# Performance work log

Hardware: AMD Instinct MI355X
Metric: run time of the kernel (lower is better)

## Reference

```python
import jax, jax.numpy as jnp
import numpy as np

T, B, H = 2048, 8, 1024


def setup_inputs() -> dict:
    key = jax.random.key(0)
    ks = jax.random.split(key, 4)
    scale = 1.0 / np.sqrt(H)
    x = jax.random.normal(ks[0], (T, B, H), dtype=jnp.float32)
    W_q = jax.random.normal(ks[1], (H, H), dtype=jnp.float32) * scale
    b_q = jnp.zeros((H,), dtype=jnp.float32)
    beta_raw = jax.random.normal(ks[2], (H,), dtype=jnp.float32)
    W_fc = jax.random.normal(ks[3], (H, H), dtype=jnp.float32) * scale
    b_fc = jnp.zeros((H,), dtype=jnp.float32)
    return {"x": x, "W_q": W_q, "b_q": b_q, "beta_raw": beta_raw,
            "W_fc": W_fc, "b_fc": b_fc}


def reference(x, W_q, b_q, beta_raw, W_fc, b_fc):
    # Per-neuron learned leak in (0,1)
    beta = jax.nn.sigmoid(beta_raw)  # (H,)
    # Input (q) projection: (T,B,H) @ (H,H)^T
    q = jnp.einsum('tbh,oh->tbo', x, W_q) + b_q  # (T,B,H)
    # Leaky integration m_t = beta * m_{t-1} + q_t as an associative scan over T
    a = jnp.broadcast_to(beta, q.shape)  # (T,B,H)

    def combine(c1, c2):
        a1, m1 = c1
        a2, m2 = c2
        return (a1 * a2, a2 * m1 + m2)

    _, m = jax.lax.associative_scan(combine, (a, q), axis=0)  # (T,B,H)
    # Linear + ReLU
    h = jnp.einsum('tbh,oh->tbo', m, W_fc) + b_fc
    return jax.nn.relu(h)
```

## Files before the change

kernel.cpp:

```cpp
#include <hip/hip_runtime.h>
#include <stdint.h>

typedef unsigned short u16;
typedef __bf16 bf16x8 __attribute__((ext_vector_type(8)));
typedef float f32x4 __attribute__((ext_vector_type(4)));

__device__ __forceinline__ u16 f2bf(float f) {
  union { float f; uint32_t u; } x; x.f = f;
  uint32_t u = x.u;
  u += 0x7fffu + ((u >> 16) & 1u);
  return (u16)(u >> 16);
}
__device__ __forceinline__ float bf2f(uint32_t lo16) {
  union { uint32_t u; float f; } x; x.u = lo16 << 16; return x.f;
}

__device__ __forceinline__ void async_load16(const u16* g, u16* l) {
  __builtin_amdgcn_global_load_lds(
      (const __attribute__((address_space(1))) void*)g,
      (__attribute__((address_space(3))) void*)l,
      16, 0, 0);
}

__global__ __launch_bounds__(256) void prep_all(const float* __restrict__ x,
                                                const float* __restrict__ Wq,
                                                const float* __restrict__ Wfc,
                                                const float* __restrict__ braw,
                                                u16* __restrict__ xb,
                                                u16* __restrict__ wqb,
                                                u16* __restrict__ wfcb,
                                                float* __restrict__ beta) {
  int gid = blockIdx.x * 256 + threadIdx.x;
  if (gid < 1024) beta[gid] = 1.0f / (1.0f + expf(-braw[gid]));
  if (gid < 131072) {
    const int HH = 1024 * 1024;
    int i = gid * 16;
    const float* src = (i < HH) ? (Wq + i) : (Wfc + (i - HH));
    u16* dst = (i < HH) ? (wqb + i) : (wfcb + (i - HH));
#pragma unroll
    for (int c = 0; c < 4; c++) {
      float4 v = *(const float4*)(src + c * 4);
      ushort4 o = {f2bf(v.x), f2bf(v.y), f2bf(v.z), f2bf(v.w)};
      *(ushort4*)(dst + c * 4) = o;
    }
  }
  {
    int i = gid * 8;
    float4 a = *(const float4*)(x + i);
    float4 b = *(const float4*)(x + i + 4);
    ushort4 o0 = {f2bf(a.x), f2bf(a.y), f2bf(a.z), f2bf(a.w)};
    ushort4 o1 = {f2bf(b.x), f2bf(b.y), f2bf(b.z), f2bf(b.w)};
    *(ushort4*)(xb + i) = o0;
    *(ushort4*)(xb + i + 4) = o1;
  }
}

template <int RELU, int OUTBF, int CARRY>
__global__ __launch_bounds__(512, 2) void gemm256(const u16* __restrict__ A,
                                                  const u16* __restrict__ B,
                                                  const float* __restrict__ bias,
                                                  void* __restrict__ Cout,
                                                  const float* __restrict__ beta_arr,
                                                  float* __restrict__ carry_out,
                                                  int M, int N, int K) {
  __shared__ u16 lds[4][2][256 * 32];

  const int tid  = threadIdx.x;
  const int lane = tid & 63;
  const int wid  = tid >> 6;
  const int wr   = (wid >> 2) * 128;
  const int wc   = (wid & 3) * 64;

  const int bid    = blockIdx.x;
  const int xcd    = bid & 7;
  const int idx    = bid >> 3;
  const int tile_m = ((xcd << 3) | (idx >> 2)) * 256;
  const int tile_n = (idx & 3) * 256;

  const int srow    = tid >> 2;
  const int schunk  = (tid & 3) ^ ((srow >> 1) & 3);
  const u16* gA = A + (size_t)(tile_m + srow) * K + schunk * 8;
  const u16* gB = B + (size_t)(tile_n + srow) * K + schunk * 8;
  const size_t half_stride = (size_t)128 * K;

#define STAGE(slot, kt)                                                   \
  do {                                                                    \
    const size_t k0 = (size_t)(kt) * 32;                                  \
    async_load16(gA + k0,               &lds[slot][0][wid * 512]);        \
    async_load16(gA + k0 + half_stride, &lds[slot][0][4096 + wid * 512]); \
    async_load16(gB + k0,               &lds[slot][1][wid * 512]);        \
    async_load16(gB + k0 + half_stride, &lds[slot][1][4096 + wid * 512]); \
  } while (0)

  f32x4 acc[8][4];
#pragma unroll
  for (int i = 0; i < 8; i++)
#pragma unroll
    for (int j = 0; j < 4; j++) acc[i][j] = (f32x4){0.f, 0.f, 0.f, 0.f};

  const int lrow = lane & 15;
  const int kq   = lane >> 4;
  const int kc   = (lrow >> 1) & 3;
  const int coff = ((kq ^ kc) << 3);

  const int NKT = K >> 5;

  STAGE(0, 0);
  if (NKT > 1) STAGE(1, 1);
  if (NKT > 2) STAGE(2, 2);
  if (NKT > 2)      asm volatile("s_waitcnt vmcnt(8)" ::: "memory");
  else if (NKT > 1) asm volatile("s_waitcnt vmcnt(4)" ::: "memory");
  else              asm volatile("s_waitcnt vmcnt(0)" ::: "memory");
  __builtin_amdgcn_s_barrier();

  for (int kt = 0; kt < NKT; ++kt) {
    const int slot = kt & 3;
    const u16* As = &lds[slot][0][0];
    const u16* Bs = &lds[slot][1][0];

    bf16x8 a[8], b[4];
#pragma unroll
    for (int i = 0; i < 8; i++)
      a[i] = *(const bf16x8*)&As[(wr + i * 16 + lrow) * 32 + coff];
#pragma unroll
    for (int j = 0; j < 4; j++)
      b[j] = *(const bf16x8*)&Bs[(wc + j * 16 + lrow) * 32 + coff];

    if (kt + 3 < NKT) STAGE((kt + 3) & 3, kt + 3);

    __builtin_amdgcn_s_setprio(1);
#pragma unroll
    for (int i = 0; i < 8; i++)
#pragma unroll
      for (int j = 0; j < 4; j++)
        acc[i][j] = __builtin_amdgcn_mfma_f32_16x16x32_bf16(a[i], b[j], acc[i][j], 0, 0, 0);
    __builtin_amdgcn_s_setprio(0);

    const int ahead = NKT - 1 - kt;
    if (ahead >= 3) {
      asm volatile("s_waitcnt vmcnt(8)" ::: "memory");
      __builtin_amdgcn_s_barrier();
    } else if (ahead == 2) {
      asm volatile("s_waitcnt vmcnt(4)" ::: "memory");
      __builtin_amdgcn_s_barrier();
    } else if (ahead == 1) {
      asm volatile("s_waitcnt vmcnt(0)" ::: "memory");
      __builtin_amdgcn_s_barrier();
    }
  }
#undef STAGE

  const int crow = (lane >> 4) << 2;
  const int ccol = lane & 15;
#pragma unroll
  for (int i = 0; i < 8; i++) {
#pragma unroll
    for (int j = 0; j < 4; j++) {
      const int gm = tile_m + wr + i * 16 + crow;
      const int gn = tile_n + wc + j * 16 + ccol;
      const float bv = bias[gn];
#pragma unroll
      for (int r = 0; r < 4; r++) {
        float v = acc[i][j][r] + bv;
        if (RELU) v = fmaxf(v, 0.f);
        if (OUTBF) ((u16*)Cout)[(size_t)(gm + r) * N + gn] = f2bf(v);
        else       ((float*)Cout)[(size_t)(gm + r) * N + gn] = v;
      }
    }
  }

  if (CARRY) {
    float* ps = (float*)&lds[0][0][0];
    const int W   = wr >> 7;
    const int kap = lane >> 5;
#pragma unroll
    for (int j = 0; j < 4; j++) {
      const int gn = tile_n + wc + j * 16 + ccol;
      const float bv = bias[gn];
      const float b1 = beta_arr[gn];
      const float b2 = b1 * b1;
      const float b4 = b2 * b2, b8 = b4 * b4, b16 = b8 * b8;
      const float scale = W ? (kap ? 1.0f : b1) : (kap ? b16 : b16 * b1);
#pragma unroll
      for (int r = 0; r < 4; r++) {
        float Hn = acc[0][j][r] + bv;
#pragma unroll
        for (int i = 1; i < 8; i++) Hn = fmaf(b2, Hn, acc[i][j][r] + bv);
        float P = scale * Hn;
        P += __shfl_xor(P, 32);
        if (lane < 32) {
          const int bb = ((lane >> 4) << 2) + r;
          ps[W * 2048 + bb * 256 + wc + j * 16 + ccol] = P;
        }
      }
    }
    __syncthreads();
    {
      const int bb = tid >> 6;
      const int h4 = (tid & 63) << 2;
      float4 lo = *(float4*)&ps[bb * 256 + h4];
      float4 hi = *(float4*)&ps[2048 + bb * 256 + h4];
      float4 s  = make_float4(lo.x + hi.x, lo.y + hi.y, lo.z + hi.z, lo.w + hi.w);
      const int seg = tile_m >> 8;
      *(float4*)&carry_out[(size_t)seg * 8192 + bb * 1024 + tile_n + h4] = s;
    }
  }
}

#define NCH 8192
#define SEG 32
#define NSEG 64

__global__ __launch_bounds__(256) void scan_fuse(const uint2* __restrict__ qb,
                                                 const float4* __restrict__ carry4,
                                                 const float* __restrict__ beta_arr,
                                                 uint2* __restrict__ mb) {
  const int tid = blockIdx.x * 256 + threadIdx.x;
  const int seg = tid >> 11;
  const int cq  = tid & 2047;
  const int h0  = (cq * 4) & 1023;
  const float b0 = beta_arr[h0], b1 = beta_arr[h0 + 1];
  const float b2 = beta_arr[h0 + 2], b3 = beta_arr[h0 + 3];
  float s0 = b0, s1 = b1, s2 = b2, s3 = b3;
#pragma unroll
  for (int i = 0; i < 5; i++) { s0 *= s0; s1 *= s1; s2 *= s2; s3 *= s3; }
  float m0 = 0.f, m1 = 0.f, m2 = 0.f, m3 = 0.f;
  const float4* cp = carry4 + cq;
  for (int s = 0; s < seg; s++) {
    float4 c = cp[(size_t)s * 2048];
    m0 = fmaf(s0, m0, c.x); m1 = fmaf(s1, m1, c.y);
    m2 = fmaf(s2, m2, c.z); m3 = fmaf(s3, m3, c.w);
  }
  const uint2* p = qb + (size_t)seg * SEG * 2048 + cq;
  uint2* o = mb + (size_t)seg * SEG * 2048 + cq;
#pragma unroll 8
  for (int t = 0; t < SEG; t++) {
    uint2 v = p[(size_t)t * 2048];
    m0 = fmaf(b0, m0, bf2f(v.x & 0xffffu));
    m1 = fmaf(b1, m1, bf2f(v.x >> 16));
    m2 = fmaf(b2, m2, bf2f(v.y & 0xffffu));
    m3 = fmaf(b3, m3, bf2f(v.y >> 16));
    uint2 w;
    w.x = (uint32_t)f2bf(m0) | ((uint32_t)f2bf(m1) << 16);
    w.y = (uint32_t)f2bf(m2) | ((uint32_t)f2bf(m3) << 16);
    o[(size_t)t * 2048] = w;
  }
}

extern "C" void kernel_launch(void* const* d_in, const int* in_sizes, int n_in,
                              void* d_out, int out_size, void* d_ws, size_t ws_size,
                              hipStream_t stream) {
  const float* x        = (const float*)d_in[0];
  const float* W_q      = (const float*)d_in[1];
  const float* b_q      = (const float*)d_in[2];
  const float* beta_raw = (const float*)d_in[3];
  const float* W_fc     = (const float*)d_in[4];
  const float* b_fc     = (const float*)d_in[5];

  const int H = 1024;
  const int M = 2048 * 8;
  const size_t MH = (size_t)M * H;

  char* ws = (char*)d_ws;
  u16* x_bf    = (u16*)ws;  ws += MH * 2;
  u16* q_bf    = (u16*)ws;  ws += MH * 2;
  u16* m_bf    = (u16*)ws;  ws += MH * 2;
  u16* wq_bf   = (u16*)ws;  ws += (size_t)H * H * 2;
  u16* wfc_bf  = (u16*)ws;  ws += (size_t)H * H * 2;
  float* beta  = (float*)ws; ws += 4096;
  float* carry = (float*)ws; ws += (size_t)NSEG * NCH * 4;

  prep_all<<<(int)(MH / 8 / 256), 256, 0, stream>>>(x, W_q, W_fc, beta_raw,
                                                    x_bf, wq_bf, wfc_bf, beta);

  gemm256<0, 1, 1><<<256, 512, 0, stream>>>(x_bf, wq_bf, b_q, q_bf,
                                            beta, carry, M, H, H);

  scan_fuse<<<NSEG * (NCH / 4) / 256, 256, 0, stream>>>((const uint2*)q_bf,
                                                        (const float4*)carry, beta,
                                                        (uint2*)m_bf);

  gemm256<1, 0, 0><<<256, 512, 0, stream>>>(m_bf, wfc_bf, b_fc, d_out,
                                            beta, nullptr, M, H, H);
}
```

Measured before the change: 234.4 us.

## Fuse local scan into first GEMM epilogue and carry fixup into second GEMM's A-load

The first GEMM now computes the within-tile leaky scan in its epilogue, using shuffles and LDS to combine the two wave-row halves, and writes segment-local m values and per-segment carries. A tiny ffold kernel turns the carries into segment prefix states. The second GEMM loads A through registers and applies the carry correction (beta^t * F) before writing to LDS. This removes the separate full-tensor scan pass over q, at the cost of a register-staged A path, extra bpow/Fbuf loads inside the GEMM main loop, and a serial 64-step fold run by only 8 blocks.

```diff
diff --git a/kernel.cpp b/kernel.cpp
--- a/kernel.cpp
+++ b/kernel.cpp
@@ -13,6 +13,15 @@
 }
 __device__ __forceinline__ float bf2f(uint32_t lo16) {
   union { uint32_t u; float f; } x; x.u = lo16 << 16; return x.f;
+}
+__device__ __forceinline__ float bfhi(uint32_t u) {
+  union { uint32_t u; float f; } x; x.u = u & 0xffff0000u; return x.f;
+}
+__device__ __forceinline__ uint32_t fixpair(uint32_t m, float p0, float p1,
+                                            float F0, float F1) {
+  float e0 = fmaf(p0, F0, bf2f(m & 0xffffu));
+  float e1 = fmaf(p1, F1, bfhi(m));
+  return (uint32_t)f2bf(e0) | ((uint32_t)f2bf(e1) << 16);
 }
 
 __device__ __forceinline__ void async_load16(const u16* g, u16* l) {
@@ -29,9 +38,16 @@
                                                 u16* __restrict__ xb,
                                                 u16* __restrict__ wqb,
                                                 u16* __restrict__ wfcb,
-                                                float* __restrict__ beta) {
+                                                float* __restrict__ beta,
+                                                float* __restrict__ bpow) {
   int gid = blockIdx.x * 256 + threadIdx.x;
-  if (gid < 1024) beta[gid] = 1.0f / (1.0f + expf(-braw[gid]));
+  if (gid < 1024) {
+    float b = 1.0f / (1.0f + expf(-braw[gid]));
+    beta[gid] = b;
+    float w = b;
+#pragma unroll 1
+    for (int p = 1; p <= 32; p++) { bpow[p * 1024 + gid] = w; w *= b; }
+  }
   if (gid < 131072) {
     const int HH = 1024 * 1024;
     int i = gid * 16;
@@ -55,14 +71,13 @@
   }
 }
 
-template <int RELU, int OUTBF, int CARRY>
-__global__ __launch_bounds__(512, 2) void gemm256(const u16* __restrict__ A,
-                                                  const u16* __restrict__ B,
-                                                  const float* __restrict__ bias,
-                                                  void* __restrict__ Cout,
-                                                  const float* __restrict__ beta_arr,
-                                                  float* __restrict__ carry_out,
-                                                  int M, int N, int K) {
+__global__ __launch_bounds__(512, 2) void gemm_scan(const u16* __restrict__ A,
+                                                    const u16* __restrict__ B,
+                                                    const float* __restrict__ bias,
+                                                    u16* __restrict__ Cout,
+                                                    const float* __restrict__ beta_arr,
+                                                    float* __restrict__ carry_out,
+                                                    int M, int N, int K) {
   __shared__ u16 lds[4][2][256 * 32];
 
   const int tid  = threadIdx.x;
@@ -152,6 +167,242 @@
 
   const int crow = (lane >> 4) << 2;
   const int ccol = lane & 15;
+  const int c4   = lane >> 4;
+  const int kap  = c4 >> 1;
+  const int Wh   = wr >> 7;
+  float* sm15 = (float*)&lds[0][0][0];
+
+#pragma unroll
+  for (int j = 0; j < 4; j++) {
+    const int gn = tile_n + wc + j * 16 + ccol;
+    const float bv = bias[gn];
+    const float be = beta_arr[gn];
+    const float be2 = be * be;
+#pragma unroll
+    for (int r = 0; r < 4; r++) {
+      float S[8], R[8];
+      S[0] = acc[0][j][r] + bv;
+#pragma unroll
+      for (int i = 1; i < 8; i++) S[i] = fmaf(be2, S[i - 1], acc[i][j][r] + bv);
+#pragma unroll
+      for (int i = 0; i < 8; i++) R[i] = __shfl_xor(S[i], 32);
+      acc[0][j][r] = kap ? fmaf(be, R[0], S[0]) : S[0];
+#pragma unroll
+      for (int i = 1; i < 8; i++)
+        acc[i][j][r] = fmaf(be, kap ? R[i] : R[i - 1], S[i]);
+    }
+  }
+  if (Wh == 0 && kap == 1) {
+#pragma unroll
+    for (int j = 0; j < 4; j++)
+#pragma unroll
+      for (int r = 0; r < 4; r++) {
+        const int bb = ((c4 << 2) + r) & 7;
+        sm15[bb * 256 + wc + j * 16 + ccol] = acc[7][j][r];
+      }
+  }
+  __syncthreads();
+  if (Wh == 1) {
+#pragma unroll
+    for (int j = 0; j < 4; j++) {
+      const int hl = wc + j * 16 + ccol;
+      const float be = beta_arr[tile_n + hl];
+      const float be2 = be * be;
+#pragma unroll
+      for (int r = 0; r < 4; r++) {
+        const int bb = ((c4 << 2) + r) & 7;
+        const float v = sm15[bb * 256 + hl];
+        float f = kap ? be2 : be;
+#pragma unroll
+        for (int i = 0; i < 8; i++) {
+          acc[i][j][r] = fmaf(f, v, acc[i][j][r]);
+          f *= be2;
+        }
+      }
+    }
+  }
+#pragma unroll
+  for (int i = 0; i < 8; i++) {
+#pragma unroll
+    for (int j = 0; j < 4; j++) {
+      const int gm = tile_m + wr + i * 16 + crow;
+      const int gn = tile_n + wc + j * 16 + ccol;
+#pragma unroll
+      for (int r = 0; r < 4; r++)
+        Cout[(size_t)(gm + r) * N + gn] = f2bf(acc[i][j][r]);
+    }
+  }
+  if (Wh == 1 && kap == 1) {
+    const int seg = tile_m >> 8;
+#pragma unroll
+    for (int j = 0; j < 4; j++) {
+      const int hl = wc + j * 16 + ccol;
+#pragma unroll
+      for (int r = 0; r < 4; r++) {
+        const int bb = ((c4 << 2) + r) & 7;
+        carry_out[(size_t)seg * 8192 + bb * 1024 + tile_n + hl] = acc[7][j][r];
+      }
+    }
+  }
+}
+
+__global__ __launch_bounds__(256) void ffold(const float4* __restrict__ carry4,
+                                             const float* __restrict__ bpow,
+                                             float4* __restrict__ Fbuf) {
+  const int cq = blockIdx.x * 256 + threadIdx.x;
+  const int hq = cq & 255;
+  const float4 b32 = *(const float4*)&bpow[32 * 1024 + hq * 4];
+  float4 F = make_float4(0.f, 0.f, 0.f, 0.f);
+  for (int s = 0; s < 64; s++) {
+    Fbuf[(size_t)s * 2048 + cq] = F;
+    float4 c = carry4[(size_t)s * 2048 + cq];
+    F.x = fmaf(b32.x, F.x, c.x);
+    F.y = fmaf(b32.y, F.y, c.y);
+    F.z = fmaf(b32.z, F.z, c.z);
+    F.w = fmaf(b32.w, F.w, c.w);
+  }
+}
+
+__global__ __launch_bounds__(512, 2) void gemm_fix(const u16* __restrict__ A,
+                                                   const u16* __restrict__ B,
+                                                   const float* __restrict__ bias,
+                                                   float* __restrict__ Cout,
+                                                   const float* __restrict__ bpow,
+                                                   const float* __restrict__ Fbuf,
+                                                   int M, int N, int K) {
+  __shared__ u16 lds[4][2][256 * 32];
+
+  const int tid  = threadIdx.x;
+  const int lane = tid & 63;
+  const int wid  = tid >> 6;
+  const int wr   = (wid >> 2) * 128;
+  const int wc   = (wid & 3) * 64;
+
+  const int bid    = blockIdx.x;
+  const int xcd    = bid & 7;
+  const int idx    = bid >> 3;
+  const int tile_m = ((xcd << 3) | (idx >> 2)) * 256;
+  const int tile_n = (idx & 3) * 256;
+
+  const int srow    = tid >> 2;
+  const int schunk  = (tid & 3) ^ ((srow >> 1) & 3);
+  const int t0      = srow >> 3;
+  const int bb      = srow & 7;
+  const int seg     = tile_m >> 8;
+
+  const u16*   gA2 = A + (size_t)(tile_m + srow) * K + schunk * 8;
+  const u16*   gB  = B + (size_t)(tile_n + srow) * K + schunk * 8;
+  const float* pb0 = bpow + (size_t)(t0 + 1) * 1024 + schunk * 8;
+  const float* fb0 = Fbuf + (size_t)seg * 8192 + bb * 1024 + schunk * 8;
+  const size_t half_stride = (size_t)128 * K;
+
+  struct ARegs { uint4 m0, m1; float4 p0l, p0h, p1l, p1h, fl, fh; };
+  ARegs rA, rB;
+
+#define STAGE_B2(slot, kt)                                                \
+  do {                                                                    \
+    const size_t k0 = (size_t)(kt) * 32;                                  \
+    async_load16(gB + k0,               &lds[slot][1][wid * 512]);        \
+    async_load16(gB + k0 + half_stride, &lds[slot][1][4096 + wid * 512]); \
+  } while (0)
+
+#define LOADA(R, kt)                                                      \
+  do {                                                                    \
+    const size_t o = (size_t)(kt) * 32;                                   \
+    (R).m0  = *(const uint4*)(gA2 + o);                                   \
+    (R).m1  = *(const uint4*)(gA2 + o + half_stride);                     \
+    (R).p0l = *(const float4*)(pb0 + o);                                  \
+    (R).p0h = *(const float4*)(pb0 + o + 4);                              \
+    (R).p1l = *(const float4*)(pb0 + o + 16384);                          \
+    (R).p1h = *(const float4*)(pb0 + o + 16388);                          \
+    (R).fl  = *(const float4*)(fb0 + o);                                  \
+    (R).fh  = *(const float4*)(fb0 + o + 4);                              \
+  } while (0)
+
+#define FIXWRITE(slot, R)                                                 \
+  do {                                                                    \
+    uint4 w0, w1;                                                         \
+    w0.x = fixpair((R).m0.x, (R).p0l.x, (R).p0l.y, (R).fl.x, (R).fl.y);   \
+    w0.y = fixpair((R).m0.y, (R).p0l.z, (R).p0l.w, (R).fl.z, (R).fl.w);   \
+    w0.z = fixpair((R).m0.z, (R).p0h.x, (R).p0h.y, (R).fh.x, (R).fh.y);   \
+    w0.w = fixpair((R).m0.w, (R).p0h.z, (R).p0h.w, (R).fh.z, (R).fh.w);   \
+    w1.x = fixpair((R).m1.x, (R).p1l.x, (R).p1l.y, (R).fl.x, (R).fl.y);   \
+    w1.y = fixpair((R).m1.y, (R).p1l.z, (R).p1l.w, (R).fl.z, (R).fl.w);   \
+    w1.z = fixpair((R).m1.z, (R).p1h.x, (R).p1h.y, (R).fh.x, (R).fh.y);   \
+    w1.w = fixpair((R).m1.w, (R).p1h.z, (R).p1h.w, (R).fh.z, (R).fh.w);   \
+    *(uint4*)&lds[slot][0][tid * 8]        = w0;                          \
+    *(uint4*)&lds[slot][0][4096 + tid * 8] = w1;                          \
+  } while (0)
+
+  f32x4 acc[8][4];
+#pragma unroll
+  for (int i = 0; i < 8; i++)
+#pragma unroll
+    for (int j = 0; j < 4; j++) acc[i][j] = (f32x4){0.f, 0.f, 0.f, 0.f};
+
+  const int lrow = lane & 15;
+  const int kq   = lane >> 4;
+  const int kc   = (lrow >> 1) & 3;
+  const int coff = ((kq ^ kc) << 3);
+
+  const int NKT = K >> 5;
+
+  LOADA(rA, 0);
+  LOADA(rB, 1);
+  STAGE_B2(0, 0);
+  STAGE_B2(1, 1);
+  STAGE_B2(2, 2);
+  asm volatile("s_waitcnt vmcnt(0)" ::: "memory");
+  FIXWRITE(0, rA);
+  FIXWRITE(1, rB);
+  LOADA(rA, 2);
+  asm volatile("s_waitcnt lgkmcnt(0)" ::: "memory");
+  __builtin_amdgcn_sched_barrier(0);
+  __builtin_amdgcn_s_barrier();
+
+#define ITER(kt, RW, RL)                                                      \
+  do {                                                                       \
+    const int slot = (kt) & 3;                                               \
+    bf16x8 a[8], b[4];                                                       \
+    _Pragma("unroll")                                                        \
+    for (int i = 0; i < 8; i++)                                              \
+      a[i] = *(const bf16x8*)&lds[slot][0][(wr + i * 16 + lrow) * 32 + coff];\
+    _Pragma("unroll")                                                        \
+    for (int j = 0; j < 4; j++)                                              \
+      b[j] = *(const bf16x8*)&lds[slot][1][(wc + j * 16 + lrow) * 32 + coff];\
+    if ((kt) + 3 < NKT) STAGE_B2(((kt) + 3) & 3, (kt) + 3);                  \
+    if ((kt) + 2 < NKT) {                                                    \
+      if ((kt) + 3 < NKT) asm volatile("s_waitcnt vmcnt(2)" ::: "memory");   \
+      else                asm volatile("s_waitcnt vmcnt(0)" ::: "memory");   \
+      FIXWRITE(((kt) + 2) & 3, RW);                                          \
+    }                                                                        \
+    if ((kt) + 3 < NKT) LOADA(RL, (kt) + 3);                                 \
+    __builtin_amdgcn_s_setprio(1);                                           \
+    _Pragma("unroll")                                                        \
+    for (int i = 0; i < 8; i++)                                              \
+      _Pragma("unroll")                                                      \
+      for (int j = 0; j < 4; j++)                                            \
+        acc[i][j] = __builtin_amdgcn_mfma_f32_16x16x32_bf16(a[i], b[j],      \
+                                                            acc[i][j], 0, 0, 0); \
+    __builtin_amdgcn_s_setprio(0);                                           \
+    if ((kt) < NKT - 1) {                                                    \
+      asm volatile("s_waitcnt lgkmcnt(0)" ::: "memory");                     \
+      __builtin_amdgcn_sched_barrier(0);                                     \
+      __builtin_amdgcn_s_barrier();                                          \
+    }                                                                        \
+  } while (0)
+
+  for (int kt = 0; kt < NKT; kt += 2) {
+    ITER(kt, rA, rB);
+    ITER(kt + 1, rB, rA);
+  }
+#undef ITER
+#undef FIXWRITE
+#undef LOADA
+#undef STAGE_B2
+
+  const int crow = (lane >> 4) << 2;
+  const int ccol = lane & 15;
 #pragma unroll
   for (int i = 0; i < 8; i++) {
 #pragma unroll
@@ -162,88 +413,10 @@
 #pragma unroll
       for (int r = 0; r < 4; r++) {
         float v = acc[i][j][r] + bv;
-        if (RELU) v = fmaxf(v, 0.f);
-        if (OUTBF) ((u16*)Cout)[(size_t)(gm + r) * N + gn] = f2bf(v);
-        else       ((float*)Cout)[(size_t)(gm + r) * N + gn] = v;
+        v = fmaxf(v, 0.f);
+        Cout[(size_t)(gm + r) * N + gn] = v;
       }
     }
-  }
-
-  if (CARRY) {
-    float* ps = (float*)&lds[0][0][0];
-    const int W   = wr >> 7;
-    const int kap = lane >> 5;
-#pragma unroll
-    for (int j = 0; j < 4; j++) {
-      const int gn = tile_n + wc + j * 16 + ccol;
-      const float bv = bias[gn];
-      const float b1 = beta_arr[gn];
-      const float b2 = b1 * b1;
-      const float b4 = b2 * b2, b8 = b4 * b4, b16 = b8 * b8;
-      const float scale = W ? (kap ? 1.0f : b1) : (kap ? b16 : b16 * b1);
-#pragma unroll
-      for (int r = 0; r < 4; r++) {
-        float Hn = acc[0][j][r] + bv;
-#pragma unroll
-        for (int i = 1; i < 8; i++) Hn = fmaf(b2, Hn, acc[i][j][r] + bv);
-        float P = scale * Hn;
-        P += __shfl_xor(P, 32);
-        if (lane < 32) {
-          const int bb = ((lane >> 4) << 2) + r;
-          ps[W * 2048 + bb * 256 + wc + j * 16 + ccol] = P;
-        }
-      }
-    }
-    __syncthreads();
-    {
-      const int bb = tid >> 6;
-      const int h4 = (tid & 63) << 2;
-      float4 lo = *(float4*)&ps[bb * 256 + h4];
-      float4 hi = *(float4*)&ps[2048 + bb * 256 + h4];
-      float4 s  = make_float4(lo.x + hi.x, lo.y + hi.y, lo.z + hi.z, lo.w + hi.w);
-      const int seg = tile_m >> 8;
-      *(float4*)&carry_out[(size_t)seg * 8192 + bb * 1024 + tile_n + h4] = s;
-    }
-  }
-}
-
-#define NCH 8192
-#define SEG 32
-#define NSEG 64
-
-__global__ __launch_bounds__(256) void scan_fuse(const uint2* __restrict__ qb,
-                                                 const float4* __restrict__ carry4,
-                                                 const float* __restrict__ beta_arr,
-                                                 uint2* __restrict__ mb) {
-  const int tid = blockIdx.x * 256 + threadIdx.x;
-  const int seg = tid >> 11;
-  const int cq  = tid & 2047;
-  const int h0  = (cq * 4) & 1023;
-  const float b0 = beta_arr[h0], b1 = beta_arr[h0 + 1];
-  const float b2 = beta_arr[h0 + 2], b3 = beta_arr[h0 + 3];
-  float s0 = b0, s1 = b1, s2 = b2, s3 = b3;
-#pragma unroll
-  for (int i = 0; i < 5; i++) { s0 *= s0; s1 *= s1; s2 *= s2; s3 *= s3; }
-  float m0 = 0.f, m1 = 0.f, m2 = 0.f, m3 = 0.f;
-  const float4* cp = carry4 + cq;
-  for (int s = 0; s < seg; s++) {
-    float4 c = cp[(size_t)s * 2048];
-    m0 = fmaf(s0, m0, c.x); m1 = fmaf(s1, m1, c.y);
-    m2 = fmaf(s2, m2, c.z); m3 = fmaf(s3, m3, c.w);
-  }
-  const uint2* p = qb + (size_t)seg * SEG * 2048 + cq;
-  uint2* o = mb + (size_t)seg * SEG * 2048 + cq;
-#pragma unroll 8
-  for (int t = 0; t < SEG; t++) {
-    uint2 v = p[(size_t)t * 2048];
-    m0 = fmaf(b0, m0, bf2f(v.x & 0xffffu));
-    m1 = fmaf(b1, m1, bf2f(v.x >> 16));
-    m2 = fmaf(b2, m2, bf2f(v.y & 0xffffu));
-    m3 = fmaf(b3, m3, bf2f(v.y >> 16));
-    uint2 w;
-    w.x = (uint32_t)f2bf(m0) | ((uint32_t)f2bf(m1) << 16);
-    w.y = (uint32_t)f2bf(m2) | ((uint32_t)f2bf(m3) << 16);
-    o[(size_t)t * 2048] = w;
   }
 }
 
@@ -263,23 +436,21 @@
 
   char* ws = (char*)d_ws;
   u16* x_bf    = (u16*)ws;  ws += MH * 2;
-  u16* q_bf    = (u16*)ws;  ws += MH * 2;
-  u16* m_bf    = (u16*)ws;  ws += MH * 2;
+  u16* m_loc   = (u16*)ws;  ws += MH * 2;
   u16* wq_bf   = (u16*)ws;  ws += (size_t)H * H * 2;
   u16* wfc_bf  = (u16*)ws;  ws += (size_t)H * H * 2;
   float* beta  = (float*)ws; ws += 4096;
-  float* carry = (float*)ws; ws += (size_t)NSEG * NCH * 4;
+  float* bpow  = (float*)ws; ws += 33 * 1024 * 4;
+  float* carry = (float*)ws; ws += (size_t)64 * 8192 * 4;
+  float* Fbuf  = (float*)ws; ws += (size_t)64 * 8192 * 4;
 
   prep_all<<<(int)(MH / 8 / 256), 256, 0, stream>>>(x, W_q, W_fc, beta_raw,
-                                                    x_bf, wq_bf, wfc_bf, beta);
-
-  gemm256<0, 1, 1><<<256, 512, 0, stream>>>(x_bf, wq_bf, b_q, q_bf,
-                                            beta, carry, M, H, H);
-
-  scan_fuse<<<NSEG * (NCH / 4) / 256, 256, 0, stream>>>((const uint2*)q_bf,
-                                                        (const float4*)carry, beta,
-                                                        (uint2*)m_bf);
-
-  gemm256<1, 0, 0><<<256, 512, 0, stream>>>(m_bf, wfc_bf, b_fc, d_out,
-                                            beta, nullptr, M, H, H);
-}
+                                                    x_bf, wq_bf, wfc_bf, beta, bpow);
+
+  gemm_scan<<<256, 512, 0, stream>>>(x_bf, wq_bf, b_q, m_loc, beta, carry, M, H, H);
+
+  ffold<<<8, 256, 0, stream>>>((const float4*)carry, bpow, (float4*)Fbuf);
+
+  gemm_fix<<<256, 512, 0, stream>>>(m_loc, wfc_bf, b_fc, (float*)d_out,
+                                    bpow, Fbuf, M, H, H);
+}
```

Result: slower. 347.8 us (+48.4%).
